# Kernel optimization log

Measured on AMD Instinct MI355X. Metric: run time of the kernel, lower is better.

The kernel has to match this reference:

```python
import jax, jax.numpy as jnp
import numpy as np

N, E, G = 50000, 400000, 64
F_IN, HID, HEADS, GF, NCLS = 16, 128, 4, 10, 6


def _init(k, shape, fan):
    return jax.random.normal(k, shape, jnp.float32) * (1.0 / np.sqrt(fan))


def setup_inputs() -> dict:
    key = jax.random.key(0)
    ks = jax.random.split(key, 16)
    x = jax.random.normal(ks[0], (N, F_IN), jnp.float32)
    edge_index = jax.random.randint(ks[1], (2, E), 0, N)
    batch = jnp.sort(jax.random.randint(ks[2], (N,), 0, G))
    graph_feat = jax.random.normal(ks[3], (G, GF), jnp.float32)
    # GATConv 1: in=16 -> heads=4, out=128, concat
    W1 = _init(ks[4], (F_IN, HEADS * HID), F_IN)
    att_src1 = _init(ks[5], (HEADS, HID), HID)
    att_dst1 = _init(ks[6], (HEADS, HID), HID)
    b1 = jnp.zeros((HEADS * HID,), jnp.float32)
    # GATConv 2: in=512 -> heads=1, out=128, mean (concat=False)
    W2 = _init(ks[7], (HEADS * HID, HID), HEADS * HID)
    att_src2 = _init(ks[8], (1, HID), HID)
    att_dst2 = _init(ks[9], (1, HID), HID)
    b2 = jnp.zeros((HID,), jnp.float32)
    # graph_proj MLP 10->32->32
    Wg1 = _init(ks[10], (GF, 32), GF); bg1 = jnp.zeros((32,), jnp.float32)
    Wg2 = _init(ks[11], (32, 32), 32); bg2 = jnp.zeros((32,), jnp.float32)
    # classifier 160->128->6
    Wc1 = _init(ks[12], (HID + 32, 128), HID + 32); bc1 = jnp.zeros((128,), jnp.float32)
    Wc2 = _init(ks[13], (128, NCLS), 128); bc2 = jnp.zeros((NCLS,), jnp.float32)
    return dict(x=x, edge_index=edge_index, batch=batch, graph_feat=graph_feat,
                W1=W1, att_src1=att_src1, att_dst1=att_dst1, b1=b1,
                W2=W2, att_src2=att_src2, att_dst2=att_dst2, b2=b2,
                Wg1=Wg1, bg1=bg1, Wg2=Wg2, bg2=bg2,
                Wc1=Wc1, bc1=bc1, Wc2=Wc2, bc2=bc2)


def gat_layer(x, W, att_src, att_dst, bias, src, dst, n_nodes, heads, out_dim, concat):
    # Linear transform: [N, H, C]
    h = (x @ W).reshape(n_nodes, heads, out_dim)
    a_src = jnp.einsum('nhc,hc->nh', h, att_src)  # [N,H]
    a_dst = jnp.einsum('nhc,hc->nh', h, att_dst)  # [N,H]
    e = jax.nn.leaky_relu(a_src[src] + a_dst[dst], 0.2)  # [Etot,H]
    # segment softmax over edges grouped by dst (self-loops ensure nonempty)
    m = jax.ops.segment_max(e, dst, num_segments=n_nodes)
    ex = jnp.exp(e - m[dst])
    denom = jax.ops.segment_sum(ex, dst, num_segments=n_nodes)
    alpha = ex / denom[dst]  # [Etot,H]
    out = jax.ops.segment_sum(alpha[:, :, None] * h[src], dst, num_segments=n_nodes)  # [N,H,C]
    if concat:
        out = out.reshape(n_nodes, heads * out_dim)
    else:
        out = out.mean(axis=1)
    return out + bias


def reference(x, edge_index, batch, graph_feat,
              W1, att_src1, att_dst1, b1,
              W2, att_src2, att_dst2, b2,
              Wg1, bg1, Wg2, bg2, Wc1, bc1, Wc2, bc2):
    n = x.shape[0]
    loops = jnp.arange(n, dtype=edge_index.dtype)
    src = jnp.concatenate([edge_index[0], loops])
    dst = jnp.concatenate([edge_index[1], loops])
    h = jax.nn.elu(gat_layer(x, W1, att_src1, att_dst1, b1, src, dst, n, HEADS, HID, True))
    h = jax.nn.elu(gat_layer(h, W2, att_src2, att_dst2, b2, src, dst, n, 1, HID, False))
    # global mean pool over graphs
    g = graph_feat.shape[0]
    sums = jax.ops.segment_sum(h, batch, num_segments=g)
    counts = jax.ops.segment_sum(jnp.ones((n, 1), h.dtype), batch, num_segments=g)
    pooled = sums / jnp.maximum(counts, 1.0)
    gf = jax.nn.relu(graph_feat @ Wg1 + bg1) @ Wg2 + bg2
    z = jnp.concatenate([pooled, gf], axis=1)
    z = jax.nn.relu(z @ Wc1 + bc1)
    return z @ Wc2 + bc2
```

## Files before the change

kernel.cpp:

```cpp
#include <hip/hip_runtime.h>
#include <hip/hip_bf16.h>

#define NN 50000
#define EE 400000
#define GG 64
#define CAP 48
#define HROW 520

typedef unsigned short u16;
typedef unsigned char u8;
typedef long long i64;
typedef unsigned long long u64;
typedef __attribute__((ext_vector_type(8))) short bf16x8;
typedef __attribute__((ext_vector_type(4))) float f32x4;
typedef __attribute__((ext_vector_type(2))) float f32x2;

__device__ __forceinline__ float b2f(u16 u) {
    unsigned int x = ((unsigned int)u) << 16;
    return __uint_as_float(x);
}
__device__ __forceinline__ u16 f2b(float f) {
    unsigned int x = __float_as_uint(f);
    unsigned int r = x + 0x7fffu + ((x >> 16) & 1u);
    return (u16)(r >> 16);
}
__device__ __forceinline__ u8 f2fp8(float f) {
    return (u8)(__builtin_amdgcn_cvt_pk_fp8_f32(f, f, 0, false) & 0xFF);
}
__device__ __forceinline__ f32x2 fp8x2_f32(unsigned int v, bool hi) {
    return hi ? __builtin_amdgcn_cvt_pk_f32_fp8(v, true)
              : __builtin_amdgcn_cvt_pk_f32_fp8(v, false);
}
__device__ __forceinline__ float wred_sum(float v) {
    #pragma unroll
    for (int o = 32; o; o >>= 1) v += __shfl_xor(v, o, 64);
    return v;
}
__device__ __forceinline__ float lrelu(float v) { return v > 0.f ? v : 0.2f * v; }

__global__ void k_prep(const int* __restrict__ batch, int* __restrict__ deg,
                       int* __restrict__ col, int* __restrict__ gstart,
                       const float* __restrict__ W1, const float* __restrict__ as1,
                       const float* __restrict__ ad1, u16* __restrict__ W1p,
                       const float* __restrict__ W2, u8* __restrict__ W2p,
                       float* __restrict__ pooled) {
    __shared__ float asw[16][8];
    int b = blockIdx.x, t = threadIdx.x;
    if (b < 196) {
        int n = b * 256 + t;
        if (n < NN) { deg[n] = 1; col[(size_t)n * CAP] = n; }
    } else if (b == 196) {
        if (t <= GG) {
            int lo = 0, hi = NN;
            while (lo < hi) {
                int mid = (lo + hi) >> 1;
                if (batch[mid] < t) lo = mid + 1; else hi = mid;
            }
            gstart[t] = lo;
        }
    } else if (b < 453) {
        int idx = (b - 197) * 256 + t;
        int j = idx & 7;
        int l = (idx >> 3) & 63;
        int ct = idx >> 9;
        int c = ct >> 3, tt = ct & 7;
        int p = c * 32 + (l >> 4) * 8 + j;
        int lp = p >> 3, jp = p & 7;
        int chan = 128 * (lp >> 4) + 16 * jp + (lp & 15);
        int n = tt * 16 + (l & 15);
        W2p[idx] = f2fp8(W2[chan * 128 + n]);
    } else if (b == 453) {
        int pair = t >> 1, half = t & 1;
        int k = pair >> 3, h = pair & 7;
        int hd = h & 3;
        const float* att = (h >= 4) ? ad1 : as1;
        float s = 0.f;
        int c0 = half * 64;
        for (int c = c0; c < c0 + 64; c++)
            s += W1[k * 512 + hd * 128 + c] * att[hd * 128 + c];
        s += __shfl_xor(s, 1, 64);
        if (half == 0) asw[k][h] = s;
        __syncthreads();
        for (int idx = t; idx < 33 * 64 * 8; idx += 256) {
            int j = idx & 7, l = (idx >> 3) & 63, tt = idx >> 9;
            int quad = l >> 4, m = l & 15;
            int k2 = quad * 8 + j;
            float v = 0.f;
            if (k2 < 16) {
                if (tt < 32) v = W1[k2 * 512 + tt * 16 + m];
                else if (m < 8) v = asw[k2][m];
            }
            W1p[idx] = f2b(v);
        }
    } else {
        for (int i = t; i < GG * 128; i += 256) pooled[i] = 0.f;
    }
}

__global__ void k_edges(const int* __restrict__ ei, int* __restrict__ deg,
                        int* __restrict__ col) {
    int e = blockIdx.x * 256 + threadIdx.x;
    if (e < EE) {
        int s = ei[e];
        int d = ei[EE + e];
        int slot = atomicAdd(&deg[d], 1);
        if (slot < CAP) col[(size_t)d * CAP + slot] = s;
    }
}

__global__ __launch_bounds__(256) void k_gemm1(
    const float* __restrict__ x, const u16* __restrict__ W1p,
    u8* __restrict__ h1, float* __restrict__ a_src1, float* __restrict__ a_dst1) {
    int tid = threadIdx.x;
    int wave = tid >> 6, l = tid & 63;
    int quad = l >> 4, m = l & 15;
    int row0 = blockIdx.x * 64 + wave * 16;
    int arow = row0 + m;
    int arow_c = arow < NN ? arow : (NN - 1);
    bf16x8 af;
    if (quad < 2) {
        const float* xp = x + arow_c * 16 + quad * 8;
        float4 x0 = *(const float4*)(xp);
        float4 x1 = *(const float4*)(xp + 4);
        u16 tmp[8] = {f2b(x0.x), f2b(x0.y), f2b(x0.z), f2b(x0.w),
                      f2b(x1.x), f2b(x1.y), f2b(x1.z), f2b(x1.w)};
        af = *(bf16x8*)tmp;
    } else {
        af = (bf16x8){0, 0, 0, 0, 0, 0, 0, 0};
    }
    const u16* bp = W1p + l * 8;
    f32x4 acc[33];
    #pragma unroll
    for (int tt = 0; tt < 33; tt++) acc[tt] = (f32x4){0.f, 0.f, 0.f, 0.f};
    #pragma unroll
    for (int tt = 0; tt < 33; tt++) {
        bf16x8 bf = *(const bf16x8*)(bp + (size_t)tt * 512);
        acc[tt] = __builtin_amdgcn_mfma_f32_16x16x32_bf16(af, bf, acc[tt], 0, 0, 0);
    }
    #pragma unroll
    for (int r = 0; r < 4; r++) {
        int row = row0 + quad * 4 + r;
        if (row >= NN) continue;
        unsigned int d[8];
        #pragma unroll
        for (int dd = 0; dd < 8; dd++) {
            unsigned int w = __builtin_amdgcn_cvt_pk_fp8_f32(acc[4 * dd][r], acc[4 * dd + 1][r], 0, false);
            w = __builtin_amdgcn_cvt_pk_fp8_f32(acc[4 * dd + 2][r], acc[4 * dd + 3][r], w, true);
            d[dd] = w;
        }
        uint4 v0; v0.x = d[0]; v0.y = d[1]; v0.z = d[2]; v0.w = d[3];
        uint4 v1; v1.x = d[4]; v1.y = d[5]; v1.z = d[6]; v1.w = d[7];
        *(uint4*)(h1 + (size_t)row * 512 + m * 32) = v0;
        *(uint4*)(h1 + (size_t)row * 512 + m * 32 + 16) = v1;
        float v = acc[32][r];
        if (m < 4) a_src1[row * 4 + m] = v;
        else if (m < 8) a_dst1[row * 4 + (m - 4)] = v;
    }
}

__global__ __launch_bounds__(1024) void k_mid(
    const int* __restrict__ deg, const int* __restrict__ col,
    const float* __restrict__ a_src1, const float* __restrict__ a_dst1,
    const u8* __restrict__ h1, const float* __restrict__ b1,
    const u8* __restrict__ W2p, const float* __restrict__ as2,
    const float* __restrict__ ad2, u8* __restrict__ hL2,
    float* __restrict__ a_src2, float* __restrict__ a_dst2) {
    __shared__ u64 hrowq[16 * HROW / 8];
    __shared__ float alphaS[16][64][4];
    __shared__ float part[16][2][8];
    u8* hrow = (u8*)hrowq;
    int t = threadIdx.x;
    int w = t >> 6, l = t & 63;
    int n0 = blockIdx.x * 16;
    int g = l >> 4, m = l & 15;
    {
        int n = n0 + w;
        int dg = min(deg[n], CAP);
        int sl = (l < dg) ? col[(size_t)n * CAP + l] : 0;
        float4 ad = *(const float4*)(a_dst1 + n * 4);
        float4 as = *(const float4*)(a_src1 + (size_t)sl * 4);
        float4 e;
        e.x = __expf(lrelu(as.x + ad.x)); e.y = __expf(lrelu(as.y + ad.y));
        e.z = __expf(lrelu(as.z + ad.z)); e.w = __expf(lrelu(as.w + ad.w));
        if (l >= dg) e = (float4){0.f, 0.f, 0.f, 0.f};
        float4 inv;
        inv.x = 1.0f / wred_sum(e.x);
        inv.y = 1.0f / wred_sum(e.y);
        inv.z = 1.0f / wred_sum(e.z);
        inv.w = 1.0f / wred_sum(e.w);
        {
            float4 a4;
            a4.x = e.x * inv.x; a4.y = e.y * inv.y;
            a4.z = e.z * inv.z; a4.w = e.w * inv.w;
            *(float4*)&alphaS[w][l][0] = a4;
        }
        const u8* hb = h1 + m * 32 + g * 8;
        f32x2 acc[4] = {{0.f, 0.f}, {0.f, 0.f}, {0.f, 0.f}, {0.f, 0.f}};
        int iters = (dg + 7) >> 3;
        for (int j = 0; j < iters; j++) {
            #pragma unroll
            for (int q = 0; q < 8; q += 2) {
                int eA = 8 * j + q, eB = 8 * j + q + 1;
                int sA = __shfl(sl, eA);
                int sB = __shfl(sl, eB);
                float aA = alphaS[w][eA][g];
                float aB = alphaS[w][eB][g];
                uint2 uA = *(const uint2*)(hb + (size_t)sA * 512);
                uint2 uB = *(const uint2*)(hb + (size_t)sB * 512);
                acc[0] += aA * fp8x2_f32(uA.x, false);
                acc[1] += aA * fp8x2_f32(uA.x, true);
                acc[2] += aA * fp8x2_f32(uA.y, false);
                acc[3] += aA * fp8x2_f32(uA.y, true);
                acc[0] += aB * fp8x2_f32(uB.x, false);
                acc[1] += aB * fp8x2_f32(uB.x, true);
                acc[2] += aB * fp8x2_f32(uB.y, false);
                acc[3] += aB * fp8x2_f32(uB.y, true);
            }
        }
        float av[8] = {acc[0].x, acc[0].y, acc[1].x, acc[1].y,
                       acc[2].x, acc[2].y, acc[3].x, acc[3].y};
        const float* bb = b1 + 128 * g + m;
        float v[8];
        #pragma unroll
        for (int j = 0; j < 8; j++) {
            float q = av[j] + bb[16 * j];
            v[j] = q > 0.f ? q : __expf(q) - 1.0f;
        }
        unsigned int d0 = __builtin_amdgcn_cvt_pk_fp8_f32(v[0], v[1], 0, false);
        d0 = __builtin_amdgcn_cvt_pk_fp8_f32(v[2], v[3], d0, true);
        unsigned int d1 = __builtin_amdgcn_cvt_pk_fp8_f32(v[4], v[5], 0, false);
        d1 = __builtin_amdgcn_cvt_pk_fp8_f32(v[6], v[7], d1, true);
        uint2 ov; ov.x = d0; ov.y = d1;
        *(uint2*)(hrow + w * HROW + l * 8) = ov;
    }
    __syncthreads();
    if (w < 8) {
        int quad = l >> 4;
        int tt = w;
        const u8* bbase = W2p + l * 8;
        f32x4 acc2 = (f32x4){0.f, 0.f, 0.f, 0.f};
        #pragma unroll
        for (int c = 0; c < 16; c++) {
            i64 af = *(const i64*)(hrow + m * HROW + c * 32 + quad * 8);
            i64 bf = *(const i64*)(bbase + (size_t)(c * 8 + tt) * 512);
            acc2 = __builtin_amdgcn_mfma_f32_16x16x32_fp8_fp8(af, bf, acc2, 0, 0, 0);
        }
        float asv = as2[tt * 16 + m], adv = ad2[tt * 16 + m];
        #pragma unroll
        for (int r = 0; r < 4; r++) {
            int node = n0 + quad * 4 + r;
            float v = acc2[r];
            hL2[(size_t)node * 128 + tt * 16 + m] = f2fp8(v);
            float rs = v * asv;
            float rd = v * adv;
            #pragma unroll
            for (int o = 1; o < 16; o <<= 1) {
                rs += __shfl_xor(rs, o, 64);
                rd += __shfl_xor(rd, o, 64);
            }
            if (m == 0) { part[quad * 4 + r][0][w] = rs; part[quad * 4 + r][1][w] = rd; }
        }
    }
    __syncthreads();
    if (t < 32) {
        int row = t >> 1, which = t & 1;
        float s = 0.f;
        #pragma unroll
        for (int i = 0; i < 8; i++) s += part[row][which][i];
        if (which) a_dst2[n0 + row] = s; else a_src2[n0 + row] = s;
    }
}

__global__ __launch_bounds__(256) void k_agg2(
    const int* __restrict__ deg, const int* __restrict__ col,
    const float* __restrict__ a_src2, const float* __restrict__ a_dst2,
    const u8* __restrict__ hL2, const float* __restrict__ b2v,
    const int* __restrict__ batch, float* __restrict__ pooled) {
    __shared__ float red[4][128];
    __shared__ int gS[4];
    int t = threadIdx.x;
    int wave = t >> 6, l = t & 63;
    int n = blockIdx.x * 4 + wave;
    if (n >= NN) return;
    int dg = min(deg[n], CAP);
    int sl = (l < dg) ? col[(size_t)n * CAP + l] : 0;
    float ad = a_dst2[n];
    float e = (l < dg) ? __expf(lrelu(a_src2[sl] + ad)) : 0.f;
    float inv = 1.0f / wred_sum(e);
    float al = e * inv;
    f32x2 acc = {0.f, 0.f};
    const u8* hb = hL2 + l * 2;
    int iters = (dg + 3) >> 2;
    for (int j = 0; j < iters; j++) {
        int e0 = 4 * j, e1 = 4 * j + 1, e2 = 4 * j + 2, e3 = 4 * j + 3;
        int s0 = __shfl(sl, e0), s1 = __shfl(sl, e1);
        int s2 = __shfl(sl, e2), s3 = __shfl(sl, e3);
        float a0 = __shfl(al, e0), a1 = __shfl(al, e1);
        float a2 = __shfl(al, e2), a3 = __shfl(al, e3);
        unsigned int u0 = *(const u16*)(hb + (size_t)s0 * 128);
        unsigned int u1 = *(const u16*)(hb + (size_t)s1 * 128);
        unsigned int u2 = *(const u16*)(hb + (size_t)s2 * 128);
        unsigned int u3 = *(const u16*)(hb + (size_t)s3 * 128);
        acc += a0 * fp8x2_f32(u0, false);
        acc += a1 * fp8x2_f32(u1, false);
        acc += a2 * fp8x2_f32(u2, false);
        acc += a3 * fp8x2_f32(u3, false);
    }
    float o0 = acc.x + b2v[2 * l];     o0 = o0 > 0.f ? o0 : __expf(o0) - 1.0f;
    float o1 = acc.y + b2v[2 * l + 1]; o1 = o1 > 0.f ? o1 : __expf(o1) - 1.0f;
    red[wave][2 * l] = o0;
    red[wave][2 * l + 1] = o1;
    if (l == 0) gS[wave] = batch[n];
    __syncthreads();
    if (t < 128) {
        int g0 = gS[0];
        if (gS[1] == g0 && gS[2] == g0 && gS[3] == g0) {
            float s = red[0][t] + red[1][t] + red[2][t] + red[3][t];
            atomicAdd(&pooled[g0 * 128 + t], s);
        } else {
            #pragma unroll
            for (int w = 0; w < 4; w++)
                atomicAdd(&pooled[gS[w] * 128 + t], red[w][t]);
        }
    }
}

__global__ __launch_bounds__(128) void k_head(
    const int* __restrict__ gstart, const float* __restrict__ pooled,
    const float* __restrict__ gfeat,
    const float* __restrict__ Wg1, const float* __restrict__ bg1,
    const float* __restrict__ Wg2, const float* __restrict__ bg2,
    const float* __restrict__ Wc1, const float* __restrict__ bc1,
    const float* __restrict__ Wc2, const float* __restrict__ bc2,
    float* __restrict__ out) {
    __shared__ float z[160];
    __shared__ float hg[32];
    __shared__ float c1b[128];
    int g = blockIdx.x, t = threadIdx.x;
    float cntf = (float)(gstart[g + 1] - gstart[g]);
    z[t] = pooled[g * 128 + t] / fmaxf(cntf, 1.0f);
    if (t < 32) {
        float a = bg1[t];
        for (int i = 0; i < 10; i++) a += gfeat[g * 10 + i] * Wg1[i * 32 + t];
        hg[t] = fmaxf(a, 0.f);
    }
    __syncthreads();
    if (t < 32) {
        float a = bg2[t];
        for (int i = 0; i < 32; i++) a += hg[i] * Wg2[i * 32 + t];
        z[128 + t] = a;
    }
    __syncthreads();
    float a = bc1[t];
    for (int i = 0; i < 160; i++) a += z[i] * Wc1[i * 128 + t];
    c1b[t] = fmaxf(a, 0.f);
    __syncthreads();
    if (t < 6) {
        float o = bc2[t];
        for (int i = 0; i < 128; i++) o += c1b[i] * Wc2[i * 6 + t];
        out[g * 6 + t] = o;
    }
}

extern "C" void kernel_launch(void* const* d_in, const int* in_sizes, int n_in,
                              void* d_out, int out_size, void* d_ws, size_t ws_size,
                              hipStream_t stream) {
    const float* x     = (const float*)d_in[0];
    const int*   ei    = (const int*)d_in[1];
    const int*   batch = (const int*)d_in[2];
    const float* gfeat = (const float*)d_in[3];
    const float* W1    = (const float*)d_in[4];
    const float* as1   = (const float*)d_in[5];
    const float* ad1   = (const float*)d_in[6];
    const float* b1    = (const float*)d_in[7];
    const float* W2    = (const float*)d_in[8];
    const float* as2   = (const float*)d_in[9];
    const float* ad2   = (const float*)d_in[10];
    const float* b2    = (const float*)d_in[11];
    const float* Wg1   = (const float*)d_in[12];
    const float* bg1   = (const float*)d_in[13];
    const float* Wg2   = (const float*)d_in[14];
    const float* bg2   = (const float*)d_in[15];
    const float* Wc1   = (const float*)d_in[16];
    const float* bc1   = (const float*)d_in[17];
    const float* Wc2   = (const float*)d_in[18];
    const float* bc2   = (const float*)d_in[19];
    float* out = (float*)d_out;

    size_t off = 0;
    char* base = (char*)d_ws;
    auto take = [&](size_t nbytes) -> char* {
        char* p = base + off;
        off = (off + nbytes + 255) & ~(size_t)255;
        return p;
    };
    u8*    h1     = (u8*)take((size_t)NN * 512);
    u8*    hL2    = (u8*)take((size_t)NN * 128);
    float* a_src1 = (float*)take((size_t)NN * 4 * 4);
    float* a_dst1 = (float*)take((size_t)NN * 4 * 4);
    float* a_src2 = (float*)take((size_t)NN * 4);
    float* a_dst2 = (float*)take((size_t)NN * 4);
    int*   deg    = (int*)take((size_t)NN * 4);
    int*   col    = (int*)take((size_t)NN * CAP * 4);
    float* pooled = (float*)take(GG * 128 * 4);
    int*   gstart = (int*)take((GG + 1) * 4);
    u8*    W2p    = (u8*)take((size_t)512 * 128);
    u16*   W1p    = (u16*)take((size_t)33 * 64 * 8 * 2);
    (void)ws_size; (void)in_sizes; (void)n_in; (void)out_size;

    k_prep<<<455, 256, 0, stream>>>(batch, deg, col, gstart, W1, as1, ad1, W1p,
                                    W2, W2p, pooled);
    k_edges<<<(EE + 255) / 256, 256, 0, stream>>>(ei, deg, col);
    k_gemm1<<<(NN + 63) / 64, 256, 0, stream>>>(x, W1p, h1, a_src1, a_dst1);
    k_mid<<<NN / 16, 1024, 0, stream>>>(deg, col, a_src1, a_dst1, h1, b1,
                                        W2p, as2, ad2, hL2, a_src2, a_dst2);
    k_agg2<<<(NN + 3) / 4, 256, 0, stream>>>(deg, col, a_src2, a_dst2, hL2, b2,
                                             batch, pooled);
    k_head<<<GG, 128, 0, stream>>>(gstart, pooled, gfeat, Wg1, bg1, Wg2, bg2,
                                   Wc1, bc1, Wc2, bc2, out);
}
```

Before: 277.0 us.

## Merge edge build into prep kernel and shrink k_mid blocks to 256 threads

Folds the edge-insertion kernel into the prep kernel and zeroes the degree array with a memset, so self-loops are added by atomic slot allocation instead of a fixed slot 0. This drops one kernel launch. k_mid moves from 1024-thread blocks to 256-thread blocks, with each wave aggregating 4 nodes in sequence and computing two MFMA output tiles, aiming at better occupancy and more work per wave. k_agg2's edge loop is unrolled by 8 to keep more gathers in flight. Edge and self-loop atomics now run in one kernel, so a self-loop may take any slot, and with CAP overflow it could be dropped.

```diff
diff --git a/kernel.cpp b/kernel.cpp
--- a/kernel.cpp
+++ b/kernel.cpp
@@ -38,18 +38,30 @@
 }
 __device__ __forceinline__ float lrelu(float v) { return v > 0.f ? v : 0.2f * v; }
 
-__global__ void k_prep(const int* __restrict__ batch, int* __restrict__ deg,
-                       int* __restrict__ col, int* __restrict__ gstart,
-                       const float* __restrict__ W1, const float* __restrict__ as1,
-                       const float* __restrict__ ad1, u16* __restrict__ W1p,
-                       const float* __restrict__ W2, u8* __restrict__ W2p,
-                       float* __restrict__ pooled) {
+__global__ void k_pe(const int* __restrict__ ei, const int* __restrict__ batch,
+                     int* __restrict__ deg, int* __restrict__ col,
+                     int* __restrict__ gstart,
+                     const float* __restrict__ W1, const float* __restrict__ as1,
+                     const float* __restrict__ ad1, u16* __restrict__ W1p,
+                     const float* __restrict__ W2, u8* __restrict__ W2p,
+                     float* __restrict__ pooled) {
     __shared__ float asw[16][8];
     int b = blockIdx.x, t = threadIdx.x;
-    if (b < 196) {
-        int n = b * 256 + t;
-        if (n < NN) { deg[n] = 1; col[(size_t)n * CAP] = n; }
-    } else if (b == 196) {
+    if (b < 1563) {
+        int e = b * 256 + t;
+        if (e < EE) {
+            int s = ei[e];
+            int d = ei[EE + e];
+            int slot = atomicAdd(&deg[d], 1);
+            if (slot < CAP) col[(size_t)d * CAP + slot] = s;
+        }
+    } else if (b < 1759) {
+        int n = (b - 1563) * 256 + t;
+        if (n < NN) {
+            int slot = atomicAdd(&deg[n], 1);
+            if (slot < CAP) col[(size_t)n * CAP + slot] = n;
+        }
+    } else if (b == 1759) {
         if (t <= GG) {
             int lo = 0, hi = NN;
             while (lo < hi) {
@@ -58,8 +70,8 @@
             }
             gstart[t] = lo;
         }
-    } else if (b < 453) {
-        int idx = (b - 197) * 256 + t;
+    } else if (b < 2016) {
+        int idx = (b - 1760) * 256 + t;
         int j = idx & 7;
         int l = (idx >> 3) & 63;
         int ct = idx >> 9;
@@ -69,7 +81,7 @@
         int chan = 128 * (lp >> 4) + 16 * jp + (lp & 15);
         int n = tt * 16 + (l & 15);
         W2p[idx] = f2fp8(W2[chan * 128 + n]);
-    } else if (b == 453) {
+    } else if (b == 2016) {
         int pair = t >> 1, half = t & 1;
         int k = pair >> 3, h = pair & 7;
         int hd = h & 3;
@@ -97,17 +109,6 @@
     }
 }
 
-__global__ void k_edges(const int* __restrict__ ei, int* __restrict__ deg,
-                        int* __restrict__ col) {
-    int e = blockIdx.x * 256 + threadIdx.x;
-    if (e < EE) {
-        int s = ei[e];
-        int d = ei[EE + e];
-        int slot = atomicAdd(&deg[d], 1);
-        if (slot < CAP) col[(size_t)d * CAP + slot] = s;
-    }
-}
-
 __global__ __launch_bounds__(256) void k_gemm1(
     const float* __restrict__ x, const u16* __restrict__ W1p,
     u8* __restrict__ h1, float* __restrict__ a_src1, float* __restrict__ a_dst1) {
@@ -158,7 +159,7 @@
     }
 }
 
-__global__ __launch_bounds__(1024) void k_mid(
+__global__ __launch_bounds__(256) void k_mid(
     const int* __restrict__ deg, const int* __restrict__ col,
     const float* __restrict__ a_src1, const float* __restrict__ a_dst1,
     const u8* __restrict__ h1, const float* __restrict__ b1,
@@ -166,15 +167,16 @@
     const float* __restrict__ ad2, u8* __restrict__ hL2,
     float* __restrict__ a_src2, float* __restrict__ a_dst2) {
     __shared__ u64 hrowq[16 * HROW / 8];
-    __shared__ float alphaS[16][64][4];
-    __shared__ float part[16][2][8];
+    __shared__ float alphaS[4][64][4];
+    __shared__ float part[16][2][4];
     u8* hrow = (u8*)hrowq;
     int t = threadIdx.x;
     int w = t >> 6, l = t & 63;
     int n0 = blockIdx.x * 16;
     int g = l >> 4, m = l & 15;
-    {
-        int n = n0 + w;
+    const u8* hb = h1 + m * 32 + g * 8;
+    for (int i = 0; i < 4; i++) {
+        int n = n0 + w * 4 + i;
         int dg = min(deg[n], CAP);
         int sl = (l < dg) ? col[(size_t)n * CAP + l] : 0;
         float4 ad = *(const float4*)(a_dst1 + n * 4);
@@ -194,7 +196,6 @@
             a4.z = e.z * inv.z; a4.w = e.w * inv.w;
             *(float4*)&alphaS[w][l][0] = a4;
         }
-        const u8* hb = h1 + m * 32 + g * 8;
         f32x2 acc[4] = {{0.f, 0.f}, {0.f, 0.f}, {0.f, 0.f}, {0.f, 0.f}};
         int iters = (dg + 7) >> 3;
         for (int j = 0; j < iters; j++) {
@@ -231,42 +232,44 @@
         unsigned int d1 = __builtin_amdgcn_cvt_pk_fp8_f32(v[4], v[5], 0, false);
         d1 = __builtin_amdgcn_cvt_pk_fp8_f32(v[6], v[7], d1, true);
         uint2 ov; ov.x = d0; ov.y = d1;
-        *(uint2*)(hrow + w * HROW + l * 8) = ov;
-    }
-    __syncthreads();
-    if (w < 8) {
-        int quad = l >> 4;
-        int tt = w;
-        const u8* bbase = W2p + l * 8;
-        f32x4 acc2 = (f32x4){0.f, 0.f, 0.f, 0.f};
+        *(uint2*)(hrow + (w * 4 + i) * HROW + l * 8) = ov;
+    }
+    __syncthreads();
+    int quad = l >> 4;
+    int tt0 = 2 * w;
+    const u8* bbase = W2p + l * 8;
+    f32x4 accA = (f32x4){0.f, 0.f, 0.f, 0.f};
+    f32x4 accB = (f32x4){0.f, 0.f, 0.f, 0.f};
+    #pragma unroll
+    for (int c = 0; c < 16; c++) {
+        i64 af = *(const i64*)(hrow + m * HROW + c * 32 + quad * 8);
+        i64 bf0 = *(const i64*)(bbase + (size_t)(c * 8 + tt0) * 512);
+        i64 bf1 = *(const i64*)(bbase + (size_t)(c * 8 + tt0 + 1) * 512);
+        accA = __builtin_amdgcn_mfma_f32_16x16x32_fp8_fp8(af, bf0, accA, 0, 0, 0);
+        accB = __builtin_amdgcn_mfma_f32_16x16x32_fp8_fp8(af, bf1, accB, 0, 0, 0);
+    }
+    float as0 = as2[tt0 * 16 + m], ad0 = ad2[tt0 * 16 + m];
+    float as1v = as2[(tt0 + 1) * 16 + m], ad1v = ad2[(tt0 + 1) * 16 + m];
+    #pragma unroll
+    for (int r = 0; r < 4; r++) {
+        int node = n0 + quad * 4 + r;
+        float v0 = accA[r], v1 = accB[r];
+        hL2[(size_t)node * 128 + tt0 * 16 + m] = f2fp8(v0);
+        hL2[(size_t)node * 128 + (tt0 + 1) * 16 + m] = f2fp8(v1);
+        float rs = v0 * as0 + v1 * as1v;
+        float rd = v0 * ad0 + v1 * ad1v;
         #pragma unroll
-        for (int c = 0; c < 16; c++) {
-            i64 af = *(const i64*)(hrow + m * HROW + c * 32 + quad * 8);
-            i64 bf = *(const i64*)(bbase + (size_t)(c * 8 + tt) * 512);
-            acc2 = __builtin_amdgcn_mfma_f32_16x16x32_fp8_fp8(af, bf, acc2, 0, 0, 0);
-        }
-        float asv = as2[tt * 16 + m], adv = ad2[tt * 16 + m];
-        #pragma unroll
-        for (int r = 0; r < 4; r++) {
-            int node = n0 + quad * 4 + r;
-            float v = acc2[r];
-            hL2[(size_t)node * 128 + tt * 16 + m] = f2fp8(v);
-            float rs = v * asv;
-            float rd = v * adv;
-            #pragma unroll
-            for (int o = 1; o < 16; o <<= 1) {
-                rs += __shfl_xor(rs, o, 64);
-                rd += __shfl_xor(rd, o, 64);
-            }
-            if (m == 0) { part[quad * 4 + r][0][w] = rs; part[quad * 4 + r][1][w] = rd; }
-        }
+        for (int o = 1; o < 16; o <<= 1) {
+            rs += __shfl_xor(rs, o, 64);
+            rd += __shfl_xor(rd, o, 64);
+        }
+        if (m == 0) { part[quad * 4 + r][0][w] = rs; part[quad * 4 + r][1][w] = rd; }
     }
     __syncthreads();
     if (t < 32) {
         int row = t >> 1, which = t & 1;
-        float s = 0.f;
-        #pragma unroll
-        for (int i = 0; i < 8; i++) s += part[row][which][i];
+        float s = part[row][which][0] + part[row][which][1] +
+                  part[row][which][2] + part[row][which][3];
         if (which) a_dst2[n0 + row] = s; else a_src2[n0 + row] = s;
     }
 }
@@ -290,21 +293,24 @@
     float al = e * inv;
     f32x2 acc = {0.f, 0.f};
     const u8* hb = hL2 + l * 2;
-    int iters = (dg + 3) >> 2;
+    int iters = (dg + 7) >> 3;
     for (int j = 0; j < iters; j++) {
-        int e0 = 4 * j, e1 = 4 * j + 1, e2 = 4 * j + 2, e3 = 4 * j + 3;
-        int s0 = __shfl(sl, e0), s1 = __shfl(sl, e1);
-        int s2 = __shfl(sl, e2), s3 = __shfl(sl, e3);
-        float a0 = __shfl(al, e0), a1 = __shfl(al, e1);
-        float a2 = __shfl(al, e2), a3 = __shfl(al, e3);
-        unsigned int u0 = *(const u16*)(hb + (size_t)s0 * 128);
-        unsigned int u1 = *(const u16*)(hb + (size_t)s1 * 128);
-        unsigned int u2 = *(const u16*)(hb + (size_t)s2 * 128);
-        unsigned int u3 = *(const u16*)(hb + (size_t)s3 * 128);
-        acc += a0 * fp8x2_f32(u0, false);
-        acc += a1 * fp8x2_f32(u1, false);
-        acc += a2 * fp8x2_f32(u2, false);
-        acc += a3 * fp8x2_f32(u3, false);
+        #pragma unroll
+        for (int q = 0; q < 8; q += 4) {
+            int e0 = 8 * j + q, e1 = e0 + 1, e2 = e0 + 2, e3 = e0 + 3;
+            int s0 = __shfl(sl, e0), s1 = __shfl(sl, e1);
+            int s2 = __shfl(sl, e2), s3 = __shfl(sl, e3);
+            float a0 = __shfl(al, e0), a1 = __shfl(al, e1);
+            float a2 = __shfl(al, e2), a3 = __shfl(al, e3);
+            unsigned int u0 = *(const u16*)(hb + (size_t)s0 * 128);
+            unsigned int u1 = *(const u16*)(hb + (size_t)s1 * 128);
+            unsigned int u2 = *(const u16*)(hb + (size_t)s2 * 128);
+            unsigned int u3 = *(const u16*)(hb + (size_t)s3 * 128);
+            acc += a0 * fp8x2_f32(u0, false);
+            acc += a1 * fp8x2_f32(u1, false);
+            acc += a2 * fp8x2_f32(u2, false);
+            acc += a3 * fp8x2_f32(u3, false);
+        }
     }
     float o0 = acc.x + b2v[2 * l];     o0 = o0 > 0.f ? o0 : __expf(o0) - 1.0f;
     float o1 = acc.y + b2v[2 * l + 1]; o1 = o1 > 0.f ? o1 : __expf(o1) - 1.0f;
@@ -408,12 +414,12 @@
     u16*   W1p    = (u16*)take((size_t)33 * 64 * 8 * 2);
     (void)ws_size; (void)in_sizes; (void)n_in; (void)out_size;
 
-    k_prep<<<455, 256, 0, stream>>>(batch, deg, col, gstart, W1, as1, ad1, W1p,
-                                    W2, W2p, pooled);
-    k_edges<<<(EE + 255) / 256, 256, 0, stream>>>(ei, deg, col);
+    hipMemsetAsync(deg, 0, (size_t)NN * 4, stream);
+    k_pe<<<2018, 256, 0, stream>>>(ei, batch, deg, col, gstart,
+                                   W1, as1, ad1, W1p, W2, W2p, pooled);
     k_gemm1<<<(NN + 63) / 64, 256, 0, stream>>>(x, W1p, h1, a_src1, a_dst1);
-    k_mid<<<NN / 16, 1024, 0, stream>>>(deg, col, a_src1, a_dst1, h1, b1,
-                                        W2p, as2, ad2, hL2, a_src2, a_dst2);
+    k_mid<<<NN / 16, 256, 0, stream>>>(deg, col, a_src1, a_dst1, h1, b1,
+                                       W2p, as2, ad2, hL2, a_src2, a_dst2);
     k_agg2<<<(NN + 3) / 4, 256, 0, stream>>>(deg, col, a_src2, a_dst2, hL2, b2,
                                              batch, pooled);
     k_head<<<GG, 128, 0, stream>>>(gstart, pooled, gfeat, Wg1, bg1, Wg2, bg2,
```

After: 250.2 us. 9.7% less time.
